# Performance work log

Measured on AMD Instinct MI355X. Metric: run time of the kernel, lower is better.

Reference implementation:

```python
import jax, jax.numpy as jnp
import numpy as np

N_NODES = 10000
N_EDGES = 80000
IN_DIM, HID, OUT_DIM, HEADS = 768, 512, 768, 4
NEG_SLOPE = 0.2


def setup_inputs() -> dict:
    key = jax.random.key(0)
    ks = jax.random.split(key, 10)
    g = 0.05
    return {
        "x": jax.random.normal(ks[0], (N_NODES, IN_DIM), jnp.float32),
        "edge_index": jax.random.randint(ks[1], (2, N_EDGES), 0, N_NODES, jnp.int64),
        # layer 1: GATConv(768 -> 512, heads=4, concat=True)
        "W1": jax.random.normal(ks[2], (IN_DIM, HEADS * HID), jnp.float32) * g,
        "a1_src": jax.random.normal(ks[3], (HEADS, HID), jnp.float32) * g,
        "a1_dst": jax.random.normal(ks[4], (HEADS, HID), jnp.float32) * g,
        "b1": jnp.zeros((HEADS * HID,), jnp.float32),
        # layer 2: GATConv(2048 -> 768, heads=1, concat=False)
        "W2": jax.random.normal(ks[5], (HEADS * HID, OUT_DIM), jnp.float32) * g,
        "a2_src": jax.random.normal(ks[6], (1, OUT_DIM), jnp.float32) * g,
        "a2_dst": jax.random.normal(ks[7], (1, OUT_DIM), jnp.float32) * g,
        "b2": jnp.zeros((OUT_DIM,), jnp.float32),
    }


def _gat_layer(x, src, dst, W, a_src, a_dst, b, heads, d_out, concat):
    N = x.shape[0]
    h = (x @ W).reshape(N, heads, d_out)              # [N, H, D]
    as_n = jnp.einsum('nhd,hd->nh', h, a_src)          # [N, H]
    ad_n = jnp.einsum('nhd,hd->nh', h, a_dst)
    e = jax.nn.leaky_relu(as_n[src] + ad_n[dst], NEG_SLOPE)  # [E, H]
    # segment softmax over destination nodes
    e_max = jax.lax.stop_gradient(jax.ops.segment_max(e, dst, num_segments=N))
    ex = jnp.exp(e - e_max[dst])
    denom = jax.ops.segment_sum(ex, dst, num_segments=N)
    alpha = ex / (denom[dst] + 1e-16)                  # [E, H]
    msg = alpha[:, :, None] * h[src]                   # [E, H, D]
    out = jax.ops.segment_sum(msg, dst, num_segments=N)  # [N, H, D]
    out = out.reshape(N, heads * d_out) if concat else out.mean(axis=1)
    return out + b


def reference(x, edge_index, W1, a1_src, a1_dst, b1, W2, a2_src, a2_dst, b2):
    N = x.shape[0]
    # PyG GATConv default: add self-loops
    loops = jnp.arange(N, dtype=edge_index.dtype)
    src = jnp.concatenate([edge_index[0], loops])
    dst = jnp.concatenate([edge_index[1], loops])
    h = _gat_layer(x, src, dst, W1, a1_src, a1_dst, b1, HEADS, HID, True)
    h = jax.nn.elu(h)
    out = _gat_layer(h, src, dst, W2, a2_src, a2_dst, b2, 1, OUT_DIM, False)
    return out
```

## Files before the change

kernel.cpp:

```cpp
#include <hip/hip_runtime.h>
#include <hip/hip_bf16.h>

#define N_NODES 10000
#define E_REAL  80000
#define E_TOTAL 90000
#define IN_DIM  768
#define HID     512
#define HEADS   4
#define OUT_DIM 768
#define HD1     (HEADS * HID)
#define NEG_SLOPE 0.2f

typedef unsigned short ushort_t;
typedef unsigned int uint_t;

__device__ inline float b2f(ushort_t u) { return __uint_as_float(((uint_t)u) << 16); }
__device__ inline ushort_t f2b(float f) {
    __hip_bfloat16 h = __float2bfloat16(f);
    return *reinterpret_cast<ushort_t*>(&h);
}

__device__ inline void edge_sd(const int* __restrict__ ei, int e, int& s, int& d) {
    if (e < E_REAL) { s = ei[e]; d = ei[E_REAL + e]; }
    else            { s = e - E_REAL; d = s; }
}

#define GLDS(g, l) __builtin_amdgcn_global_load_lds( \
    (const __attribute__((address_space(1))) void*)(g), \
    (__attribute__((address_space(3))) void*)(l), 16, 0, 0)

static const long B_H1B  = 0L;
static const long B_HB   = 40960000L;
static const long B_XB   = 81920000L;
static const long B_W1T  = 97280000L;
static const long B_W2T  = 100425728L;
static const long B_SM   = 103571456L;
static const long SM_AS1   = 0;
static const long SM_AD1   = 40000;
static const long SM_DEN1  = 120000;
static const long SM_E1    = 160000;
static const long SM_AS2   = 520000;
static const long SM_AD2   = 530000;
static const long SM_DEN2  = 550000;
static const long SM_E2    = 560000;
static const long SM_CNT   = 650000;
static const long SM_ROWS  = 660000;
static const long SM_CURS  = 670016;
static const long SM_END   = 680032;
static const long B_CSRS = B_SM + SM_END * 4;
static const long B_CSRE = B_CSRS + 360000L;

__global__ __launch_bounds__(256)
void cast_bf16(const float* __restrict__ in, ushort_t* __restrict__ o, long n) {
    long i = ((long)blockIdx.x * 256 + threadIdx.x) * 8;
    if (i >= n) return;
    float4 v0 = *(const float4*)(in + i);
    float4 v1 = *(const float4*)(in + i + 4);
    ushort_t r[8] = {f2b(v0.x), f2b(v0.y), f2b(v0.z), f2b(v0.w),
                     f2b(v1.x), f2b(v1.y), f2b(v1.z), f2b(v1.w)};
    *(uint4*)(o + i) = *(uint4*)r;
}

__global__ __launch_bounds__(256)
void cast_transpose(const float* __restrict__ W, ushort_t* __restrict__ WT,
                    int K, int N) {
    __shared__ ushort_t t[32][33];
    const int n0 = blockIdx.x * 32, k0 = blockIdx.y * 32;
    const int tx = threadIdx.x & 31, ty = threadIdx.x >> 5;
#pragma unroll
    for (int i = 0; i < 4; ++i) {
        int k = ty + i * 8;
        t[k][tx] = f2b(W[(long)(k0 + k) * N + n0 + tx]);
    }
    __syncthreads();
#pragma unroll
    for (int i = 0; i < 4; ++i) {
        int n = ty + i * 8;
        WT[(long)(n0 + n) * K + k0 + tx] = t[tx][n];
    }
}

typedef short bf16x8 __attribute__((ext_vector_type(8)));
typedef float f32x4 __attribute__((ext_vector_type(4)));

#define BM 128
#define BN 128
#define BK 32

__global__ __launch_bounds__(256)
void gemm_bf16(const ushort_t* __restrict__ A, const ushort_t* __restrict__ BT,
               ushort_t* __restrict__ C, int M, int N, int K) {
    __shared__ ushort_t As[BM * BK];
    __shared__ ushort_t Bs[BN * BK];
    const int tid  = threadIdx.x;
    const int wave = tid >> 6, lane = tid & 63;
    const int quad = lane >> 4, l16 = lane & 15;
    const int bm = blockIdx.y * BM, bn = blockIdx.x * BN;
    const int wr = (wave >> 1) * 64, wc = (wave & 1) * 64;

    const int ch0 = wave * 128 + lane;
    const int ch1 = ch0 + 64;
    const int r0 = ch0 >> 2, c0 = (ch0 & 3) ^ ((r0 >> 1) & 3);
    const int r1 = ch1 >> 2, c1 = (ch1 & 3) ^ ((r1 >> 1) & 3);
    const ushort_t* a0 = A + (long)(bm + r0) * K + c0 * 8;
    const ushort_t* a1 = A + (long)(bm + r1) * K + c1 * 8;
    const ushort_t* b0 = BT + (long)(bn + r0) * K + c0 * 8;
    const ushort_t* b1 = BT + (long)(bn + r1) * K + c1 * 8;
    ushort_t* lA0 = As + (wave * 128) * 8;
    ushort_t* lA1 = As + (wave * 128 + 64) * 8;
    ushort_t* lB0 = Bs + (wave * 128) * 8;
    ushort_t* lB1 = Bs + (wave * 128 + 64) * 8;

    const int swz = (l16 >> 1) & 3;
    f32x4 acc[4][4] = {};

    for (int k0 = 0; k0 < K; k0 += BK) {
        GLDS(a0 + k0, lA0);
        GLDS(a1 + k0, lA1);
        GLDS(b0 + k0, lB0);
        GLDS(b1 + k0, lB1);
        __syncthreads();
        bf16x8 af[4], bfr[4];
#pragma unroll
        for (int i = 0; i < 4; ++i) {
            af[i]  = *(const bf16x8*)(As + ((wr + i * 16 + l16) * 4 + (quad ^ swz)) * 8);
            bfr[i] = *(const bf16x8*)(Bs + ((wc + i * 16 + l16) * 4 + (quad ^ swz)) * 8);
        }
#pragma unroll
        for (int i = 0; i < 4; ++i)
#pragma unroll
            for (int j = 0; j < 4; ++j)
                acc[i][j] = __builtin_amdgcn_mfma_f32_16x16x32_bf16(
                    af[i], bfr[j], acc[i][j], 0, 0, 0);
        __syncthreads();
    }

#pragma unroll
    for (int i = 0; i < 4; ++i) {
#pragma unroll
        for (int r = 0; r < 4; ++r) {
            int row = bm + wr + i * 16 + quad * 4 + r;
            if (row >= M) continue;
#pragma unroll
            for (int j = 0; j < 4; ++j) {
                int col = bn + wc + j * 16 + l16;
                C[(long)row * N + col] = f2b(acc[i][j][r]);
            }
        }
    }
}

__global__ __launch_bounds__(256)
void attn1(const ushort_t* __restrict__ h, const float* __restrict__ a_s,
           const float* __restrict__ a_d, float* __restrict__ os,
           float* __restrict__ od) {
    const int n = blockIdx.x;
    const int w = threadIdx.x >> 6, lane = threadIdx.x & 63;
    uint4 hv = *(const uint4*)(h + (long)n * HD1 + w * HID + lane * 8);
    const float* asp = a_s + w * HID + lane * 8;
    const float* adp = a_d + w * HID + lane * 8;
    const ushort_t* pb = (const ushort_t*)&hv;
    float ps = 0.f, pd = 0.f;
#pragma unroll
    for (int c = 0; c < 8; ++c) {
        float v = b2f(pb[c]);
        ps += v * asp[c];
        pd += v * adp[c];
    }
#pragma unroll
    for (int off = 32; off > 0; off >>= 1) {
        ps += __shfl_down(ps, off);
        pd += __shfl_down(pd, off);
    }
    if (lane == 0) { os[n * HEADS + w] = ps; od[n * HEADS + w] = pd; }
}

__global__ __launch_bounds__(256)
void attn2(const ushort_t* __restrict__ h, const float* __restrict__ a_s,
           const float* __restrict__ a_d, float* __restrict__ os,
           float* __restrict__ od) {
    __shared__ float rs[4], rd[4];
    const int n = blockIdx.x, tid = threadIdx.x;
    const int w = tid >> 6, lane = tid & 63;
    float ps = 0.f, pd = 0.f;
#pragma unroll
    for (int j = 0; j < 3; ++j) {
        int c = tid + j * 256;
        float v = b2f(h[(long)n * OUT_DIM + c]);
        ps += v * a_s[c];
        pd += v * a_d[c];
    }
#pragma unroll
    for (int off = 32; off > 0; off >>= 1) {
        ps += __shfl_down(ps, off);
        pd += __shfl_down(pd, off);
    }
    if (lane == 0) { rs[w] = ps; rd[w] = pd; }
    __syncthreads();
    if (tid == 0) {
        os[n] = rs[0] + rs[1] + rs[2] + rs[3];
        od[n] = rd[0] + rd[1] + rd[2] + rd[3];
    }
}

__global__ __launch_bounds__(256)
void edge_soft(const int* __restrict__ ei, int H,
               const float* __restrict__ as_n, const float* __restrict__ ad_n,
               float* __restrict__ ebuf, float* __restrict__ denom) {
    int idx = blockIdx.x * 256 + threadIdx.x;
    if (idx >= E_TOTAL * H) return;
    int e = idx / H, hh = idx - e * H;
    int s, d; edge_sd(ei, e, s, d);
    float v = as_n[(long)s * H + hh] + ad_n[(long)d * H + hh];
    v = v > 0.f ? v : NEG_SLOPE * v;
    float ex = expf(v);
    ebuf[idx] = ex;
    atomicAdd(&denom[(long)d * H + hh], ex);
}

__global__ __launch_bounds__(256)
void hist_dst(const int* __restrict__ ei, int* __restrict__ cnt) {
    int e = blockIdx.x * 256 + threadIdx.x;
    if (e >= E_TOTAL) return;
    int s, d; edge_sd(ei, e, s, d);
    atomicAdd(&cnt[d], 1);
}

#define SCAN_CH 40
__global__ __launch_bounds__(256)
void scan_nodes(const int* __restrict__ cnt, int* __restrict__ rows,
                int* __restrict__ curs) {
    __shared__ int part[256];
    const int tid = threadIdx.x;
    const int base = tid * SCAN_CH;
    int local[SCAN_CH];
    int sum = 0;
#pragma unroll
    for (int i = 0; i < SCAN_CH; ++i) {
        int idx = base + i;
        int v = (idx < N_NODES) ? cnt[idx] : 0;
        local[i] = v; sum += v;
    }
    part[tid] = sum;
    __syncthreads();
    for (int off = 1; off < 256; off <<= 1) {
        int v = (tid >= off) ? part[tid - off] : 0;
        __syncthreads();
        part[tid] += v;
        __syncthreads();
    }
    int run = part[tid] - sum;
#pragma unroll
    for (int i = 0; i < SCAN_CH; ++i) {
        int idx = base + i;
        if (idx < N_NODES) { rows[idx] = run; curs[idx] = run; run += local[i]; }
    }
    if (tid == 255) rows[N_NODES] = run;
}

__global__ __launch_bounds__(256)
void scatter_edges(const int* __restrict__ ei, int* __restrict__ curs,
                   int* __restrict__ csr_src, int* __restrict__ csr_eid) {
    int e = blockIdx.x * 256 + threadIdx.x;
    if (e >= E_TOTAL) return;
    int s, d; edge_sd(ei, e, s, d);
    int pos = atomicAdd(&curs[d], 1);
    csr_src[pos] = s;
    csr_eid[pos] = e;
}

__global__ __launch_bounds__(256)
void agg1(const int* __restrict__ rows, const int* __restrict__ csr_src,
          const int* __restrict__ csr_eid, const float* __restrict__ ebuf,
          const float* __restrict__ denom, const ushort_t* __restrict__ hf,
          const float* __restrict__ b1, ushort_t* __restrict__ o) {
    const int n = blockIdx.x, tid = threadIdx.x;
    const int beg = rows[n], end = rows[n + 1];
    const int hh = tid >> 6;
    const float dinv = 1.f / (denom[(long)n * HEADS + hh] + 1e-16f);
    float acc[8] = {};
    for (int k = beg; k < end; k += 4) {
        int nk = end - k; if (nk > 4) nk = 4;
        uint4 v[4]; float al[4];
#pragma unroll
        for (int u = 0; u < 4; ++u) {
            if (u < nk) {
                int s = csr_src[k + u];
                al[u] = ebuf[(long)csr_eid[k + u] * HEADS + hh] * dinv;
                v[u]  = *(const uint4*)(hf + (long)s * HD1 + tid * 8);
            }
        }
#pragma unroll
        for (int u = 0; u < 4; ++u) {
            if (u < nk) {
                const ushort_t* p = (const ushort_t*)&v[u];
#pragma unroll
                for (int c = 0; c < 8; ++c) acc[c] += al[u] * b2f(p[c]);
            }
        }
    }
    ushort_t r[8];
#pragma unroll
    for (int c = 0; c < 8; ++c) {
        float vv = acc[c] + b1[tid * 8 + c];
        r[c] = f2b(vv > 0.f ? vv : expm1f(vv));
    }
    *(uint4*)(o + (long)n * HD1 + tid * 8) = *(uint4*)r;
}

__global__ __launch_bounds__(256)
void agg2(const int* __restrict__ rows, const int* __restrict__ csr_src,
          const int* __restrict__ csr_eid, const float* __restrict__ ebuf,
          const float* __restrict__ denom, const ushort_t* __restrict__ hf,
          const float* __restrict__ b2, float* __restrict__ out) {
    const int n = blockIdx.x, tid = threadIdx.x;
    const int beg = rows[n], end = rows[n + 1];
    const float dinv = 1.f / (denom[n] + 1e-16f);
    float a0 = 0.f, a1 = 0.f, a2 = 0.f;
    for (int k = beg; k < end; k += 4) {
        int nk = end - k; if (nk > 4) nk = 4;
        float al[4]; ushort_t v0[4], v1[4], v2[4];
#pragma unroll
        for (int u = 0; u < 4; ++u) {
            if (u < nk) {
                int s = csr_src[k + u];
                al[u] = ebuf[csr_eid[k + u]] * dinv;
                const ushort_t* hp = hf + (long)s * OUT_DIM;
                v0[u] = hp[tid]; v1[u] = hp[tid + 256]; v2[u] = hp[tid + 512];
            }
        }
#pragma unroll
        for (int u = 0; u < 4; ++u) {
            if (u < nk) {
                a0 += al[u] * b2f(v0[u]);
                a1 += al[u] * b2f(v1[u]);
                a2 += al[u] * b2f(v2[u]);
            }
        }
    }
    float* op = out + (long)n * OUT_DIM;
    op[tid]       = a0 + b2[tid];
    op[tid + 256] = a1 + b2[tid + 256];
    op[tid + 512] = a2 + b2[tid + 512];
}

extern "C" void kernel_launch(void* const* d_in, const int* in_sizes, int n_in,
                              void* d_out, int out_size, void* d_ws, size_t ws_size,
                              hipStream_t stream) {
    const float* x   = (const float*)d_in[0];
    const int*   ei  = (const int*)d_in[1];
    const float* W1  = (const float*)d_in[2];
    const float* a1s = (const float*)d_in[3];
    const float* a1d = (const float*)d_in[4];
    const float* b1  = (const float*)d_in[5];
    const float* W2  = (const float*)d_in[6];
    const float* a2s = (const float*)d_in[7];
    const float* a2d = (const float*)d_in[8];
    const float* b2  = (const float*)d_in[9];
    float* out = (float*)d_out;
    char* base = (char*)d_ws;

    ushort_t* h1b = (ushort_t*)(base + B_H1B);
    ushort_t* hb  = (ushort_t*)(base + B_HB);
    ushort_t* xb  = (ushort_t*)(base + B_XB);
    ushort_t* h2b = xb;
    ushort_t* w1t = (ushort_t*)(base + B_W1T);
    ushort_t* w2t = (ushort_t*)(base + B_W2T);
    float*    sm  = (float*)(base + B_SM);

    float* as1  = sm + SM_AS1;
    float* ad1  = sm + SM_AD1;
    float* den1 = sm + SM_DEN1;
    float* e1   = sm + SM_E1;
    float* as2  = sm + SM_AS2;
    float* ad2  = sm + SM_AD2;
    float* den2 = sm + SM_DEN2;
    float* e2   = sm + SM_E2;
    int* cnt    = (int*)(sm + SM_CNT);
    int* rows   = (int*)(sm + SM_ROWS);
    int* curs   = (int*)(sm + SM_CURS);
    int* csr_src = (int*)(base + B_CSRS);
    int* csr_eid = (int*)(base + B_CSRE);

    hipMemsetAsync(sm, 0, (size_t)(SM_CNT + 10000) * sizeof(float), stream);

    {
        long nx = (long)N_NODES * IN_DIM;
        cast_bf16<<<(int)(nx / 8 / 256 + 1), 256, 0, stream>>>(x, xb, nx);
        cast_transpose<<<dim3(HD1 / 32, IN_DIM / 32), 256, 0, stream>>>(W1, w1t, IN_DIM, HD1);
        cast_transpose<<<dim3(OUT_DIM / 32, HD1 / 32), 256, 0, stream>>>(W2, w2t, HD1, OUT_DIM);
        hist_dst<<<(E_TOTAL + 255) / 256, 256, 0, stream>>>(ei, cnt);
        scan_nodes<<<1, 256, 0, stream>>>(cnt, rows, curs);
        scatter_edges<<<(E_TOTAL + 255) / 256, 256, 0, stream>>>(ei, curs, csr_src, csr_eid);
    }

    gemm_bf16<<<dim3(HD1 / BN, (N_NODES + BM - 1) / BM), 256, 0, stream>>>(
        xb, w1t, h1b, N_NODES, HD1, IN_DIM);
    attn1<<<N_NODES, 256, 0, stream>>>(h1b, a1s, a1d, as1, ad1);
    {
        int total = E_TOTAL * HEADS;
        edge_soft<<<(total + 255) / 256, 256, 0, stream>>>(ei, HEADS, as1, ad1, e1, den1);
    }
    agg1<<<N_NODES, 256, 0, stream>>>(rows, csr_src, csr_eid, e1, den1, h1b, b1, hb);

    gemm_bf16<<<dim3(OUT_DIM / BN, (N_NODES + BM - 1) / BM), 256, 0, stream>>>(
        hb, w2t, h2b, N_NODES, OUT_DIM, HD1);
    attn2<<<N_NODES, 256, 0, stream>>>(h2b, a2s, a2d, as2, ad2);
    {
        int total = E_TOTAL;
        edge_soft<<<(total + 255) / 256, 256, 0, stream>>>(ei, 1, as2, ad2, e2, den2);
    }
    agg2<<<N_NODES, 256, 0, stream>>>(rows, csr_src, csr_eid, e2, den2, h2b, b2, out);
}
```

Before: 383.1 us.

## Store layer-1 features head-major and split aggregation into per-head single-wave blocks

The first GEMM now writes its output head-major ([head][node][HID]), so each head's slice is a contiguous 10000x512 array. agg1 launches one 64-thread block per (node, head) and gathers only that head's 1 KB row, which is meant to improve cache locality for the random gathers. agg2 becomes a single-wave block that uses 16-byte and 8-byte vector loads instead of scalar ushort loads. The GEMM epilogue's scattered head-major store pattern and the larger number of small blocks may add overhead.

```diff
diff --git a/kernel.cpp b/kernel.cpp
--- a/kernel.cpp
+++ b/kernel.cpp
@@ -10,6 +10,7 @@
 #define OUT_DIM 768
 #define HD1     (HEADS * HID)
 #define NEG_SLOPE 0.2f
+#define H1_HSTRIDE (N_NODES * HID)
 
 typedef unsigned short ushort_t;
 typedef unsigned int uint_t;
@@ -87,6 +88,7 @@
 #define BN 128
 #define BK 32
 
+template<int CMODE>
 __global__ __launch_bounds__(256)
 void gemm_bf16(const ushort_t* __restrict__ A, const ushort_t* __restrict__ BT,
                ushort_t* __restrict__ C, int M, int N, int K) {
@@ -144,7 +146,12 @@
 #pragma unroll
             for (int j = 0; j < 4; ++j) {
                 int col = bn + wc + j * 16 + l16;
-                C[(long)row * N + col] = f2b(acc[i][j][r]);
+                if (CMODE == 0) {
+                    C[(long)row * N + col] = f2b(acc[i][j][r]);
+                } else {
+                    C[(long)(col >> 9) * H1_HSTRIDE + (long)row * HID + (col & 511)]
+                        = f2b(acc[i][j][r]);
+                }
             }
         }
     }
@@ -156,7 +163,7 @@
            float* __restrict__ od) {
     const int n = blockIdx.x;
     const int w = threadIdx.x >> 6, lane = threadIdx.x & 63;
-    uint4 hv = *(const uint4*)(h + (long)n * HD1 + w * HID + lane * 8);
+    uint4 hv = *(const uint4*)(h + (long)w * H1_HSTRIDE + (long)n * HID + lane * 8);
     const float* asp = a_s + w * HID + lane * 8;
     const float* adp = a_d + w * HID + lane * 8;
     const ushort_t* pb = (const ushort_t*)&hv;
@@ -269,14 +276,14 @@
     csr_eid[pos] = e;
 }
 
-__global__ __launch_bounds__(256)
+__global__ __launch_bounds__(64)
 void agg1(const int* __restrict__ rows, const int* __restrict__ csr_src,
           const int* __restrict__ csr_eid, const float* __restrict__ ebuf,
           const float* __restrict__ denom, const ushort_t* __restrict__ hf,
           const float* __restrict__ b1, ushort_t* __restrict__ o) {
-    const int n = blockIdx.x, tid = threadIdx.x;
+    const int n = blockIdx.x, hh = blockIdx.y, lane = threadIdx.x;
     const int beg = rows[n], end = rows[n + 1];
-    const int hh = tid >> 6;
+    const ushort_t* hsl = hf + (long)hh * H1_HSTRIDE;
     const float dinv = 1.f / (denom[(long)n * HEADS + hh] + 1e-16f);
     float acc[8] = {};
     for (int k = beg; k < end; k += 4) {
@@ -287,7 +294,7 @@
             if (u < nk) {
                 int s = csr_src[k + u];
                 al[u] = ebuf[(long)csr_eid[k + u] * HEADS + hh] * dinv;
-                v[u]  = *(const uint4*)(hf + (long)s * HD1 + tid * 8);
+                v[u]  = *(const uint4*)(hsl + (long)s * HID + lane * 8);
             }
         }
 #pragma unroll
@@ -299,49 +306,56 @@
             }
         }
     }
+    const float* bp = b1 + hh * HID + lane * 8;
     ushort_t r[8];
 #pragma unroll
     for (int c = 0; c < 8; ++c) {
-        float vv = acc[c] + b1[tid * 8 + c];
+        float vv = acc[c] + bp[c];
         r[c] = f2b(vv > 0.f ? vv : expm1f(vv));
     }
-    *(uint4*)(o + (long)n * HD1 + tid * 8) = *(uint4*)r;
-}
-
-__global__ __launch_bounds__(256)
+    *(uint4*)(o + (long)n * HD1 + hh * HID + lane * 8) = *(uint4*)r;
+}
+
+__global__ __launch_bounds__(64)
 void agg2(const int* __restrict__ rows, const int* __restrict__ csr_src,
           const int* __restrict__ csr_eid, const float* __restrict__ ebuf,
           const float* __restrict__ denom, const ushort_t* __restrict__ hf,
           const float* __restrict__ b2, float* __restrict__ out) {
-    const int n = blockIdx.x, tid = threadIdx.x;
+    const int n = blockIdx.x, lane = threadIdx.x;
     const int beg = rows[n], end = rows[n + 1];
     const float dinv = 1.f / (denom[n] + 1e-16f);
-    float a0 = 0.f, a1 = 0.f, a2 = 0.f;
+    float acc[12] = {};
     for (int k = beg; k < end; k += 4) {
         int nk = end - k; if (nk > 4) nk = 4;
-        float al[4]; ushort_t v0[4], v1[4], v2[4];
+        uint4 v4[4]; uint2 v2[4]; float al[4];
 #pragma unroll
         for (int u = 0; u < 4; ++u) {
             if (u < nk) {
                 int s = csr_src[k + u];
                 al[u] = ebuf[csr_eid[k + u]] * dinv;
                 const ushort_t* hp = hf + (long)s * OUT_DIM;
-                v0[u] = hp[tid]; v1[u] = hp[tid + 256]; v2[u] = hp[tid + 512];
+                v4[u] = *(const uint4*)(hp + lane * 8);
+                v2[u] = *(const uint2*)(hp + 512 + lane * 4);
             }
         }
 #pragma unroll
         for (int u = 0; u < 4; ++u) {
             if (u < nk) {
-                a0 += al[u] * b2f(v0[u]);
-                a1 += al[u] * b2f(v1[u]);
-                a2 += al[u] * b2f(v2[u]);
+                const ushort_t* p4 = (const ushort_t*)&v4[u];
+                const ushort_t* p2 = (const ushort_t*)&v2[u];
+#pragma unroll
+                for (int c = 0; c < 8; ++c) acc[c] += al[u] * b2f(p4[c]);
+#pragma unroll
+                for (int c = 0; c < 4; ++c) acc[8 + c] += al[u] * b2f(p2[c]);
             }
         }
     }
     float* op = out + (long)n * OUT_DIM;
-    op[tid]       = a0 + b2[tid];
-    op[tid + 256] = a1 + b2[tid + 256];
-    op[tid + 512] = a2 + b2[tid + 512];
+#pragma unroll
+    for (int c = 0; c < 8; ++c) op[lane * 8 + c] = acc[c] + b2[lane * 8 + c];
+#pragma unroll
+    for (int c = 0; c < 4; ++c)
+        op[512 + lane * 4 + c] = acc[8 + c] + b2[512 + lane * 4 + c];
 }
 
 extern "C" void kernel_launch(void* const* d_in, const int* in_sizes, int n_in,
@@ -394,21 +408,21 @@
         scatter_edges<<<(E_TOTAL + 255) / 256, 256, 0, stream>>>(ei, curs, csr_src, csr_eid);
     }
 
-    gemm_bf16<<<dim3(HD1 / BN, (N_NODES + BM - 1) / BM), 256, 0, stream>>>(
+    gemm_bf16<1><<<dim3(HD1 / BN, (N_NODES + BM - 1) / BM), 256, 0, stream>>>(
         xb, w1t, h1b, N_NODES, HD1, IN_DIM);
     attn1<<<N_NODES, 256, 0, stream>>>(h1b, a1s, a1d, as1, ad1);
     {
         int total = E_TOTAL * HEADS;
         edge_soft<<<(total + 255) / 256, 256, 0, stream>>>(ei, HEADS, as1, ad1, e1, den1);
     }
-    agg1<<<N_NODES, 256, 0, stream>>>(rows, csr_src, csr_eid, e1, den1, h1b, b1, hb);
-
-    gemm_bf16<<<dim3(OUT_DIM / BN, (N_NODES + BM - 1) / BM), 256, 0, stream>>>(
+    agg1<<<dim3(N_NODES, HEADS), 64, 0, stream>>>(rows, csr_src, csr_eid, e1, den1, h1b, b1, hb);
+
+    gemm_bf16<0><<<dim3(OUT_DIM / BN, (N_NODES + BM - 1) / BM), 256, 0, stream>>>(
         hb, w2t, h2b, N_NODES, OUT_DIM, HD1);
     attn2<<<N_NODES, 256, 0, stream>>>(h2b, a2s, a2d, as2, ad2);
     {
         int total = E_TOTAL;
         edge_soft<<<(total + 255) / 256, 256, 0, stream>>>(ei, 1, as2, ad2, e2, den2);
     }
-    agg2<<<N_NODES, 256, 0, stream>>>(rows, csr_src, csr_eid, e2, den2, h2b, b2, out);
-}
+    agg2<<<N_NODES, 64, 0, stream>>>(rows, csr_src, csr_eid, e2, den2, h2b, b2, out);
+}
```

Measured after the change: 364.8 us. -4.8%, faster.
